# Kernel optimization log

Hardware: AMD Instinct MI355X
Metric: run time of the kernel (lower is better)

## Reference

```python
import jax, jax.numpy as jnp
import numpy as np

N_NODES = 50000
N_EDGES = 800000
DIN, EIN, DOUT, EOUT, H = 64, 32, 64, 64, 128


def mlp(x, W1, b1, W2, b2):
    # Linear -> ReLU -> Linear (assumed MLP definition, hidden=128)
    return jnp.dot(jax.nn.relu(jnp.dot(x, W1) + b1), W2) + b2


def setup_inputs() -> dict:
    key = jax.random.key(0)
    ks = jax.random.split(key, 18)
    init = lambda k, shape: (jax.random.normal(k, shape, dtype=jnp.float32)
                             / np.float32(np.sqrt(shape[0])))
    em_in = 2 * DIN + EIN   # 160
    nm_in = DIN + EOUT      # 128
    return {
        "nf": jax.random.normal(ks[0], (N_NODES, DIN), dtype=jnp.float32),
        "ef": jax.random.normal(ks[1], (N_EDGES, EIN), dtype=jnp.float32),
        "src": jax.random.randint(ks[2], (N_EDGES,), 0, N_NODES, dtype=jnp.int32),
        "dst": jax.random.randint(ks[3], (N_EDGES,), 0, N_NODES, dtype=jnp.int32),
        # edge model MLP
        "We1": init(ks[4], (em_in, H)), "be1": jnp.zeros((H,), jnp.float32),
        "We2": init(ks[5], (H, EOUT)), "be2": jnp.zeros((EOUT,), jnp.float32),
        # attention model MLP (scalar logit per edge)
        "Wa1": init(ks[6], (em_in, H)), "ba1": jnp.zeros((H,), jnp.float32),
        "Wa2": init(ks[7], (H, 1)), "ba2": jnp.zeros((1,), jnp.float32),
        # node model MLP
        "Wn1": init(ks[8], (nm_in, H)), "bn1": jnp.zeros((H,), jnp.float32),
        "Wn2": init(ks[9], (H, DOUT)), "bn2": jnp.zeros((DOUT,), jnp.float32),
    }


def reference(nf, ef, src, dst, We1, be1, We2, be2, Wa1, ba1, Wa2, ba2,
              Wn1, bn1, Wn2, bn2):
    # per-edge gather + concat: [E, 2*DIN + EIN]
    e_in = jnp.concatenate([nf[src], nf[dst], ef], axis=-1)
    uh_e = mlp(e_in, We1, be1, We2, be2)          # [E, EOUT]
    logits = mlp(e_in, Wa1, ba1, Wa2, ba2)        # [E, 1]
    # edge softmax over incoming edges of each destination node
    m = jax.ops.segment_max(logits, dst, num_segments=N_NODES)
    m = jnp.where(jnp.isfinite(m), m, jnp.float32(0.0))
    ex = jnp.exp(logits - m[dst])
    denom = jax.ops.segment_sum(ex, dst, num_segments=N_NODES)
    attn = ex / jnp.maximum(denom[dst], jnp.float32(1e-38))  # [E, 1]
    # attention-weighted scatter-sum aggregation
    agg = jax.ops.segment_sum(uh_e * attn, dst, num_segments=N_NODES)  # [N, EOUT]
    # node update MLP on concat(agg_m, nf)
    uh_n = mlp(jnp.concatenate([agg, nf], axis=-1), Wn1, bn1, Wn2, bn2)
    return (uh_n, uh_e)
```

## Files before the change

kernel.cpp:

```cpp
#include <hip/hip_runtime.h>


typedef unsigned short u16;
typedef __attribute__((ext_vector_type(8))) short bf16x8;
typedef __attribute__((ext_vector_type(4))) float f32x4;

#define NN 50000
#define NE 800000

__device__ __forceinline__ u16 f2bf(float f){
  union { float f; unsigned int i; } v; v.f = f;
  unsigned int i = v.i;
  return (u16)((i + 0x7FFFu + ((i >> 16) & 1u)) >> 16);
}
__device__ __forceinline__ uint2 f4tobf(float4 f){
  uint2 p;
  p.x = (unsigned)f2bf(f.x) | ((unsigned)f2bf(f.y) << 16);
  p.y = (unsigned)f2bf(f.z) | ((unsigned)f2bf(f.w) << 16);
  return p;
}

__global__ void prep_kernel(const float* __restrict__ We1, const float* __restrict__ Wa1,
                            const float* __restrict__ We2, const float* __restrict__ Wa2,
                            const float* __restrict__ Wn1, const float* __restrict__ Wn2,
                            u16* __restrict__ w1t, u16* __restrict__ w2t,
                            u16* __restrict__ wn1t, u16* __restrict__ wn2t,
                            int* __restrict__ head)
{
  int i = blockIdx.x * 256 + threadIdx.x;
  if (i < 40960) {
    int n = i / 160, k = i % 160;
    w1t[i] = f2bf((n < 128) ? We1[k*128 + n] : Wa1[k*128 + (n-128)]);
  } else if (i < 51200) {
    int j = i - 40960; int n = j / 128, k = j % 128;
    float v = (n < 64) ? We2[k*64 + n] : ((n == 64) ? Wa2[k] : 0.f);
    w2t[j] = f2bf(v);
  } else if (i < 67584) {
    int j = i - 51200; int n = j / 128, k = j % 128;
    wn1t[j] = f2bf(Wn1[k*128 + n]);
  } else if (i < 75776) {
    int j = i - 67584; int n = j / 128, k = j % 128;
    wn2t[j] = f2bf(Wn2[k*64 + n]);
  } else if (i < 125776) {
    head[i - 75776] = -1;
  }
}

__global__ void nfbf_kernel(const float* __restrict__ nf, u16* __restrict__ nfb)
{
  int i = blockIdx.x * 256 + threadIdx.x;
  if (i >= NN * 16) return;
  float4 f = *(const float4*)(nf + (size_t)i * 4);
  *(uint2*)&nfb[(size_t)i * 4] = f4tobf(f);
}

__global__ void link_kernel(const int* __restrict__ dst, int* __restrict__ head,
                            int* __restrict__ nxt)
{
  int e = blockIdx.x * 256 + threadIdx.x;
  if (e >= NE) return;
  nxt[e] = atomicExch(&head[dst[e]], e);
}

__global__ __launch_bounds__(256, 4) void edge_kernel(
    const u16* __restrict__ nfb, const float* __restrict__ ef,
    const int* __restrict__ src, const int* __restrict__ dst,
    const u16* __restrict__ w1t, const u16* __restrict__ w2t,
    const float* __restrict__ be1, const float* __restrict__ ba1,
    const float* __restrict__ be2, const float* __restrict__ ba2,
    float* __restrict__ uh_e, float* __restrict__ exu)
{
  __shared__ u16 smem[16896];
  __shared__ int s_src[64], s_dst[64];
  u16* eins = smem;
  u16* hsm  = smem;
  float* outs = (float*)smem;

  const int t = threadIdx.x;
  const int base = blockIdx.x * 64;

  if (t < 64)        s_src[t]      = src[base + t];
  else if (t < 128)  s_dst[t - 64] = dst[base + (t - 64)];
  __syncthreads();

  #pragma unroll
  for (int i = 0; i < 4; i++) {
    int idx = i*256 + t;
    int e = idx >> 4, c = idx & 15;
    uint2 v = *(const uint2*)(nfb + (size_t)s_src[e]*64 + c*4);
    *(uint2*)&eins[e*168 + c*4] = v;
  }
  #pragma unroll
  for (int i = 0; i < 4; i++) {
    int idx = i*256 + t;
    int e = idx >> 4, c = idx & 15;
    uint2 v = *(const uint2*)(nfb + (size_t)s_dst[e]*64 + c*4);
    *(uint2*)&eins[e*168 + 64 + c*4] = v;
  }
  #pragma unroll
  for (int i = 0; i < 2; i++) {
    int idx = i*256 + t;
    int e = idx >> 3, c = idx & 7;
    float4 f = *(const float4*)(ef + (size_t)(base + e)*32 + c*4);
    *(uint2*)&eins[e*168 + 128 + c*4] = f4tobf(f);
  }
  __syncthreads();

  const int lane = t & 63, wave = t >> 6;
  const int r = lane & 15, quad = lane >> 4;

  f32x4 acc[4][4];
  #pragma unroll
  for (int rf = 0; rf < 4; rf++)
    #pragma unroll
    for (int j = 0; j < 4; j++) acc[rf][j] = {0.f, 0.f, 0.f, 0.f};

  #pragma unroll
  for (int k0 = 0; k0 < 160; k0 += 32) {
    bf16x8 a[4];
    #pragma unroll
    for (int rf = 0; rf < 4; rf++)
      a[rf] = *(const bf16x8*)&eins[(rf*16 + r)*168 + k0 + quad*8];
    #pragma unroll
    for (int j = 0; j < 4; j++) {
      bf16x8 b = *(const bf16x8*)(w1t + (size_t)((wave*4 + j)*16 + r)*160 + k0 + quad*8);
      #pragma unroll
      for (int rf = 0; rf < 4; rf++)
        acc[rf][j] = __builtin_amdgcn_mfma_f32_16x16x32_bf16(a[rf], b, acc[rf][j], 0, 0, 0);
    }
  }
  __syncthreads();

  #pragma unroll
  for (int j = 0; j < 4; j++) {
    int col = (wave*4 + j)*16 + r;
    float bias = (wave < 2) ? be1[col] : ba1[col - 128];
    #pragma unroll
    for (int rf = 0; rf < 4; rf++)
      #pragma unroll
      for (int i = 0; i < 4; i++) {
        float h = fmaxf(acc[rf][j][i] + bias, 0.f);
        hsm[(rf*16 + quad*4 + i)*264 + col] = f2bf(h);
      }
  }
  __syncthreads();

  f32x4 acc2[4];
  f32x4 accl = {0.f, 0.f, 0.f, 0.f};
  #pragma unroll
  for (int rf = 0; rf < 4; rf++) acc2[rf] = {0.f, 0.f, 0.f, 0.f};

  #pragma unroll
  for (int k0 = 0; k0 < 128; k0 += 32) {
    bf16x8 bw = *(const bf16x8*)(w2t + (size_t)(wave*16 + r)*128 + k0 + quad*8);
    #pragma unroll
    for (int rf = 0; rf < 4; rf++) {
      bf16x8 ae = *(const bf16x8*)&hsm[(rf*16 + r)*264 + k0 + quad*8];
      acc2[rf] = __builtin_amdgcn_mfma_f32_16x16x32_bf16(ae, bw, acc2[rf], 0, 0, 0);
    }
    bf16x8 al = *(const bf16x8*)&hsm[(wave*16 + r)*264 + 128 + k0 + quad*8];
    bf16x8 bl = *(const bf16x8*)(w2t + (size_t)(64 + r)*128 + k0 + quad*8);
    accl = __builtin_amdgcn_mfma_f32_16x16x32_bf16(al, bl, accl, 0, 0, 0);
  }
  __syncthreads();

  {
    int col = wave*16 + r;
    float bias = be2[col];
    #pragma unroll
    for (int rf = 0; rf < 4; rf++)
      #pragma unroll
      for (int i = 0; i < 4; i++)
        outs[(rf*16 + quad*4 + i)*64 + col] = acc2[rf][i] + bias;
  }
  if (r == 0) {
    float bias = ba2[0];
    #pragma unroll
    for (int i = 0; i < 4; i++) {
      int row = wave*16 + quad*4 + i;
      float x = __expf(fminf(fmaxf(accl[i] + bias, -50.f), 50.f));
      exu[base + row] = x;
    }
  }
  __syncthreads();

  #pragma unroll
  for (int i = 0; i < 4; i++) {
    int idx = i*256 + t;
    int row = idx >> 4, c = idx & 15;
    *(float4*)(uh_e + (size_t)(base + row)*64 + c*4) = *(const float4*)&outs[row*64 + c*4];
  }
}

__global__ void agg_kernel(const int* __restrict__ head, const int* __restrict__ nxt,
                           const float* __restrict__ exu,
                           const float* __restrict__ uh_e, float* __restrict__ aggf)
{
  int gid = blockIdx.x * 256 + threadIdx.x;
  int v = gid >> 6, lane = gid & 63;
  if (v >= NN) return;
  float acc = 0.f, s = 0.f;
  int e = head[v];
  while (e >= 0) {
    float x = exu[e];
    s += x;
    acc += x * uh_e[(size_t)e*64 + lane];
    e = nxt[e];
  }
  aggf[(size_t)v*64 + lane] = acc / fmaxf(s, 1e-38f);
}

__global__ __launch_bounds__(256, 4) void node_kernel(
    const float* __restrict__ aggf, const float* __restrict__ nf,
    const u16* __restrict__ wn1t, const u16* __restrict__ wn2t,
    const float* __restrict__ bn1, const float* __restrict__ bn2,
    float* __restrict__ uh_n)
{
  __shared__ u16 smem[8704];
  u16* xs = smem;
  float* outs = (float*)smem;

  const int t = threadIdx.x;
  const int base = blockIdx.x * 64;

  #pragma unroll
  for (int i = 0; i < 8; i++) {
    int idx = i*256 + t;
    int row = idx >> 5, c = idx & 31;
    int v = base + row;
    float4 f = {0.f, 0.f, 0.f, 0.f};
    if (v < NN) {
      if (c < 16) f = *(const float4*)(aggf + (size_t)v*64 + c*4);
      else        f = *(const float4*)(nf   + (size_t)v*64 + (c-16)*4);
    }
    *(uint2*)&xs[row*136 + c*4] = f4tobf(f);
  }
  __syncthreads();

  const int lane = t & 63, wave = t >> 6;
  const int r = lane & 15, quad = lane >> 4;

  f32x4 acc1[8];
  #pragma unroll
  for (int i = 0; i < 8; i++) acc1[i] = {0.f, 0.f, 0.f, 0.f};
  #pragma unroll
  for (int k0 = 0; k0 < 128; k0 += 32) {
    bf16x8 a = *(const bf16x8*)&xs[(wave*16 + r)*136 + k0 + quad*8];
    #pragma unroll
    for (int tt = 0; tt < 8; tt++) {
      bf16x8 b = *(const bf16x8*)(wn1t + (size_t)(tt*16 + r)*128 + k0 + quad*8);
      acc1[tt] = __builtin_amdgcn_mfma_f32_16x16x32_bf16(a, b, acc1[tt], 0, 0, 0);
    }
  }
  __syncthreads();

  u16* hb = smem + wave*(16*136);
  #pragma unroll
  for (int tt = 0; tt < 8; tt++) {
    int col = tt*16 + r;
    float bias = bn1[col];
    #pragma unroll
    for (int i = 0; i < 4; i++) {
      float h = fmaxf(acc1[tt][i] + bias, 0.f);
      hb[(quad*4 + i)*136 + col] = f2bf(h);
    }
  }
  __syncthreads();

  f32x4 acc2[4];
  #pragma unroll
  for (int i = 0; i < 4; i++) acc2[i] = {0.f, 0.f, 0.f, 0.f};
  #pragma unroll
  for (int k0 = 0; k0 < 128; k0 += 32) {
    bf16x8 a = *(const bf16x8*)&hb[r*136 + k0 + quad*8];
    #pragma unroll
    for (int tt = 0; tt < 4; tt++) {
      bf16x8 b = *(const bf16x8*)(wn2t + (size_t)(tt*16 + r)*128 + k0 + quad*8);
      acc2[tt] = __builtin_amdgcn_mfma_f32_16x16x32_bf16(a, b, acc2[tt], 0, 0, 0);
    }
  }
  __syncthreads();

  #pragma unroll
  for (int tt = 0; tt < 4; tt++) {
    int col = tt*16 + r;
    float bias = bn2[col];
    #pragma unroll
    for (int i = 0; i < 4; i++)
      outs[(wave*16 + quad*4 + i)*64 + col] = acc2[tt][i] + bias;
  }
  __syncthreads();

  #pragma unroll
  for (int i = 0; i < 4; i++) {
    int idx = i*256 + t;
    int row = idx >> 4, c = idx & 15;
    int v2 = base + row;
    if (v2 < NN)
      *(float4*)(uh_n + (size_t)v2*64 + c*4) = *(const float4*)&outs[row*64 + c*4];
  }
}

extern "C" void kernel_launch(void* const* d_in, const int* in_sizes, int n_in,
                              void* d_out, int out_size, void* d_ws, size_t ws_size,
                              hipStream_t stream)
{
  const float* nf  = (const float*)d_in[0];
  const float* ef  = (const float*)d_in[1];
  const int*   src = (const int*)d_in[2];
  const int*   dst = (const int*)d_in[3];
  const float* We1 = (const float*)d_in[4];
  const float* be1 = (const float*)d_in[5];
  const float* We2 = (const float*)d_in[6];
  const float* be2 = (const float*)d_in[7];
  const float* Wa1 = (const float*)d_in[8];
  const float* ba1 = (const float*)d_in[9];
  const float* Wa2 = (const float*)d_in[10];
  const float* ba2 = (const float*)d_in[11];
  const float* Wn1 = (const float*)d_in[12];
  const float* bn1 = (const float*)d_in[13];
  const float* Wn2 = (const float*)d_in[14];
  const float* bn2 = (const float*)d_in[15];

  char* ws = (char*)d_ws;
  u16*   w1t    = (u16*)  (ws + 0);
  u16*   w2t    = (u16*)  (ws + 81920);
  u16*   wn1t   = (u16*)  (ws + 102400);
  u16*   wn2t   = (u16*)  (ws + 135168);
  float* exu    = (float*)(ws + 151552);
  int*   head   = (int*)  (ws + 3551552);
  int*   nxt    = (int*)  (ws + 3751552);

  float* uh_n = (float*)d_out;
  float* uh_e = (float*)d_out + (size_t)NN * 64;
  u16*   nfb  = (u16*)d_out;
  float* aggf = uh_n;

  prep_kernel<<<492, 256, 0, stream>>>(We1, Wa1, We2, Wa2, Wn1, Wn2,
                                       w1t, w2t, wn1t, wn2t, head);
  nfbf_kernel<<<3125, 256, 0, stream>>>(nf, nfb);
  link_kernel<<<(NE + 255)/256, 256, 0, stream>>>(dst, head, nxt);
  edge_kernel<<<NE/64, 256, 0, stream>>>(nfb, ef, src, dst, w1t, w2t,
                                         be1, ba1, be2, ba2, uh_e, exu);
  agg_kernel<<<(NN*64)/256, 256, 0, stream>>>(head, nxt, exu, uh_e, aggf);
  node_kernel<<<(NN + 63)/64, 256, 0, stream>>>(aggf, nf, wn1t, wn2t, bn1, bn2, uh_n);
}
```

Before: 649.7 us.

## Replace linked-list edge grouping with CSR build and persistent weight-resident edge kernel

```diff
diff --git a/kernel.cpp b/kernel.cpp
--- a/kernel.cpp
+++ b/kernel.cpp
@@ -25,7 +25,7 @@
                             const float* __restrict__ Wn1, const float* __restrict__ Wn2,
                             u16* __restrict__ w1t, u16* __restrict__ w2t,
                             u16* __restrict__ wn1t, u16* __restrict__ wn2t,
-                            int* __restrict__ head)
+                            int* __restrict__ deg)
 {
   int i = blockIdx.x * 256 + threadIdx.x;
   if (i < 40960) {
@@ -42,27 +42,69 @@
     int j = i - 67584; int n = j / 128, k = j % 128;
     wn2t[j] = f2bf(Wn2[k*64 + n]);
   } else if (i < 125776) {
-    head[i - 75776] = -1;
-  }
-}
-
-__global__ void nfbf_kernel(const float* __restrict__ nf, u16* __restrict__ nfb)
+    deg[i - 75776] = 0;
+  }
+}
+
+__global__ void deg_nfbf_kernel(const float* __restrict__ nf, u16* __restrict__ nfb,
+                                const int* __restrict__ dst, int* __restrict__ deg)
 {
   int i = blockIdx.x * 256 + threadIdx.x;
-  if (i >= NN * 16) return;
+  if (i >= NE) return;
   float4 f = *(const float4*)(nf + (size_t)i * 4);
   *(uint2*)&nfb[(size_t)i * 4] = f4tobf(f);
-}
-
-__global__ void link_kernel(const int* __restrict__ dst, int* __restrict__ head,
-                            int* __restrict__ nxt)
+  atomicAdd(&deg[dst[i]], 1);
+}
+
+__global__ void scan1_kernel(const int* __restrict__ deg, int* __restrict__ part,
+                             int* __restrict__ bsum)
+{
+  __shared__ int sm[256];
+  int t = threadIdx.x, g = blockIdx.x * 256 + t;
+  int x = (g < NN) ? deg[g] : 0;
+  sm[t] = x; __syncthreads();
+  #pragma unroll
+  for (int o = 1; o < 256; o <<= 1) {
+    int y = (t >= o) ? sm[t - o] : 0; __syncthreads();
+    sm[t] += y; __syncthreads();
+  }
+  if (g < NN) part[g] = sm[t] - x;
+  if (t == 255) bsum[blockIdx.x] = sm[255];
+}
+
+__global__ void scan2_kernel(int* __restrict__ bsum)
+{
+  __shared__ int sm[256];
+  int t = threadIdx.x;
+  int x = (t < 196) ? bsum[t] : 0;
+  sm[t] = x; __syncthreads();
+  #pragma unroll
+  for (int o = 1; o < 256; o <<= 1) {
+    int y = (t >= o) ? sm[t - o] : 0; __syncthreads();
+    sm[t] += y; __syncthreads();
+  }
+  if (t < 196) bsum[t] = sm[t] - x;
+}
+
+__global__ void scan3_kernel(const int* __restrict__ part, const int* __restrict__ bsum,
+                             int* __restrict__ rowptr, int* __restrict__ cursor)
+{
+  int g = blockIdx.x * 256 + threadIdx.x;
+  if (g >= NN) return;
+  int r = part[g] + bsum[blockIdx.x];
+  rowptr[g] = r; cursor[g] = r;
+}
+
+__global__ void fill_kernel(const int* __restrict__ dst, int* __restrict__ cursor,
+                            int* __restrict__ csr_e)
 {
   int e = blockIdx.x * 256 + threadIdx.x;
   if (e >= NE) return;
-  nxt[e] = atomicExch(&head[dst[e]], e);
-}
-
-__global__ __launch_bounds__(256, 4) void edge_kernel(
+  int slot = atomicAdd(&cursor[dst[e]], 1);
+  csr_e[slot] = e;
+}
+
+__global__ __launch_bounds__(256, 2) void edge_kernel(
     const u16* __restrict__ nfb, const float* __restrict__ ef,
     const int* __restrict__ src, const int* __restrict__ dst,
     const u16* __restrict__ w1t, const u16* __restrict__ w2t,
@@ -70,142 +112,162 @@
     const float* __restrict__ be2, const float* __restrict__ ba2,
     float* __restrict__ uh_e, float* __restrict__ exu)
 {
-  __shared__ u16 smem[16896];
-  __shared__ int s_src[64], s_dst[64];
-  u16* eins = smem;
-  u16* hsm  = smem;
-  float* outs = (float*)smem;
+  __shared__ u16 eins[64*168];
+  __shared__ u16 hsm [64*264];
+  __shared__ float outs[64*64];
 
   const int t = threadIdx.x;
-  const int base = blockIdx.x * 64;
-
-  if (t < 64)        s_src[t]      = src[base + t];
-  else if (t < 128)  s_dst[t - 64] = dst[base + (t - 64)];
-  __syncthreads();
-
-  #pragma unroll
-  for (int i = 0; i < 4; i++) {
-    int idx = i*256 + t;
-    int e = idx >> 4, c = idx & 15;
-    uint2 v = *(const uint2*)(nfb + (size_t)s_src[e]*64 + c*4);
-    *(uint2*)&eins[e*168 + c*4] = v;
-  }
-  #pragma unroll
-  for (int i = 0; i < 4; i++) {
-    int idx = i*256 + t;
-    int e = idx >> 4, c = idx & 15;
-    uint2 v = *(const uint2*)(nfb + (size_t)s_dst[e]*64 + c*4);
-    *(uint2*)&eins[e*168 + 64 + c*4] = v;
-  }
-  #pragma unroll
-  for (int i = 0; i < 2; i++) {
-    int idx = i*256 + t;
-    int e = idx >> 3, c = idx & 7;
-    float4 f = *(const float4*)(ef + (size_t)(base + e)*32 + c*4);
-    *(uint2*)&eins[e*168 + 128 + c*4] = f4tobf(f);
-  }
-  __syncthreads();
-
   const int lane = t & 63, wave = t >> 6;
   const int r = lane & 15, quad = lane >> 4;
 
-  f32x4 acc[4][4];
-  #pragma unroll
-  for (int rf = 0; rf < 4; rf++)
-    #pragma unroll
-    for (int j = 0; j < 4; j++) acc[rf][j] = {0.f, 0.f, 0.f, 0.f};
-
-  #pragma unroll
-  for (int k0 = 0; k0 < 160; k0 += 32) {
-    bf16x8 a[4];
-    #pragma unroll
-    for (int rf = 0; rf < 4; rf++)
-      a[rf] = *(const bf16x8*)&eins[(rf*16 + r)*168 + k0 + quad*8];
-    #pragma unroll
-    for (int j = 0; j < 4; j++) {
-      bf16x8 b = *(const bf16x8*)(w1t + (size_t)((wave*4 + j)*16 + r)*160 + k0 + quad*8);
-      #pragma unroll
-      for (int rf = 0; rf < 4; rf++)
-        acc[rf][j] = __builtin_amdgcn_mfma_f32_16x16x32_bf16(a[rf], b, acc[rf][j], 0, 0, 0);
-    }
-  }
-  __syncthreads();
-
+  bf16x8 wv1[5][4];
+  #pragma unroll
+  for (int k = 0; k < 5; k++)
+    #pragma unroll
+    for (int j = 0; j < 4; j++)
+      wv1[k][j] = *(const bf16x8*)(w1t + (size_t)((wave*4 + j)*16 + r)*160 + k*32 + quad*8);
+  bf16x8 wv2[4], wvl[4];
+  #pragma unroll
+  for (int k = 0; k < 4; k++) {
+    wv2[k] = *(const bf16x8*)(w2t + (size_t)(wave*16 + r)*128 + k*32 + quad*8);
+    wvl[k] = *(const bf16x8*)(w2t + (size_t)(64 + r)*128 + k*32 + quad*8);
+  }
+  float bias1[4];
   #pragma unroll
   for (int j = 0; j < 4; j++) {
     int col = (wave*4 + j)*16 + r;
-    float bias = (wave < 2) ? be1[col] : ba1[col - 128];
+    bias1[j] = (col < 128) ? be1[col] : ba1[col - 128];
+  }
+  const float bias2 = be2[wave*16 + r];
+  const float biasl = ba2[0];
+
+  for (int tt0 = 0; tt0 < 8; tt0++) {
+    int tile = blockIdx.x * 8 + tt0;
+    if (tile >= NE/64) break;
+    const int base = tile * 64;
+
+    #pragma unroll
+    for (int i = 0; i < 4; i++) {
+      int idx = i*256 + t;
+      int e = idx >> 4, c = idx & 15;
+      int sv = src[base + e];
+      *(uint2*)&eins[e*168 + c*4] = *(const uint2*)(nfb + (size_t)sv*64 + c*4);
+    }
+    #pragma unroll
+    for (int i = 0; i < 4; i++) {
+      int idx = i*256 + t;
+      int e = idx >> 4, c = idx & 15;
+      int dv = dst[base + e];
+      *(uint2*)&eins[e*168 + 64 + c*4] = *(const uint2*)(nfb + (size_t)dv*64 + c*4);
+    }
+    #pragma unroll
+    for (int i = 0; i < 2; i++) {
+      int idx = i*256 + t;
+      int e = idx >> 3, c = idx & 7;
+      float4 f = *(const float4*)(ef + (size_t)(base + e)*32 + c*4);
+      *(uint2*)&eins[e*168 + 128 + c*4] = f4tobf(f);
+    }
+    __syncthreads();
+
+    f32x4 acc[4][4];
     #pragma unroll
     for (int rf = 0; rf < 4; rf++)
       #pragma unroll
+      for (int j = 0; j < 4; j++) acc[rf][j] = {0.f, 0.f, 0.f, 0.f};
+
+    #pragma unroll
+    for (int k = 0; k < 5; k++) {
+      bf16x8 a[4];
+      #pragma unroll
+      for (int rf = 0; rf < 4; rf++)
+        a[rf] = *(const bf16x8*)&eins[(rf*16 + r)*168 + k*32 + quad*8];
+      #pragma unroll
+      for (int j = 0; j < 4; j++)
+        #pragma unroll
+        for (int rf = 0; rf < 4; rf++)
+          acc[rf][j] = __builtin_amdgcn_mfma_f32_16x16x32_bf16(a[rf], wv1[k][j], acc[rf][j], 0, 0, 0);
+    }
+
+    #pragma unroll
+    for (int j = 0; j < 4; j++) {
+      int col = (wave*4 + j)*16 + r;
+      #pragma unroll
+      for (int rf = 0; rf < 4; rf++)
+        #pragma unroll
+        for (int i = 0; i < 4; i++) {
+          float h = fmaxf(acc[rf][j][i] + bias1[j], 0.f);
+          hsm[(rf*16 + quad*4 + i)*264 + col] = f2bf(h);
+        }
+    }
+    __syncthreads();
+
+    f32x4 acc2[4];
+    f32x4 accl = {0.f, 0.f, 0.f, 0.f};
+    #pragma unroll
+    for (int rf = 0; rf < 4; rf++) acc2[rf] = {0.f, 0.f, 0.f, 0.f};
+    #pragma unroll
+    for (int k = 0; k < 4; k++) {
+      #pragma unroll
+      for (int rf = 0; rf < 4; rf++) {
+        bf16x8 ae = *(const bf16x8*)&hsm[(rf*16 + r)*264 + k*32 + quad*8];
+        acc2[rf] = __builtin_amdgcn_mfma_f32_16x16x32_bf16(ae, wv2[k], acc2[rf], 0, 0, 0);
+      }
+      bf16x8 al = *(const bf16x8*)&hsm[(wave*16 + r)*264 + 128 + k*32 + quad*8];
+      accl = __builtin_amdgcn_mfma_f32_16x16x32_bf16(al, wvl[k], accl, 0, 0, 0);
+    }
+
+    {
+      int col = wave*16 + r;
+      #pragma unroll
+      for (int rf = 0; rf < 4; rf++)
+        #pragma unroll
+        for (int i = 0; i < 4; i++)
+          outs[(rf*16 + quad*4 + i)*64 + col] = acc2[rf][i] + bias2;
+    }
+    if (r == 0) {
+      #pragma unroll
       for (int i = 0; i < 4; i++) {
-        float h = fmaxf(acc[rf][j][i] + bias, 0.f);
-        hsm[(rf*16 + quad*4 + i)*264 + col] = f2bf(h);
+        int row = wave*16 + quad*4 + i;
+        float x = __expf(fminf(fmaxf(accl[i] + biasl, -50.f), 50.f));
+        exu[base + row] = x;
       }
-  }
-  __syncthreads();
-
-  f32x4 acc2[4];
-  f32x4 accl = {0.f, 0.f, 0.f, 0.f};
-  #pragma unroll
-  for (int rf = 0; rf < 4; rf++) acc2[rf] = {0.f, 0.f, 0.f, 0.f};
-
-  #pragma unroll
-  for (int k0 = 0; k0 < 128; k0 += 32) {
-    bf16x8 bw = *(const bf16x8*)(w2t + (size_t)(wave*16 + r)*128 + k0 + quad*8);
-    #pragma unroll
-    for (int rf = 0; rf < 4; rf++) {
-      bf16x8 ae = *(const bf16x8*)&hsm[(rf*16 + r)*264 + k0 + quad*8];
-      acc2[rf] = __builtin_amdgcn_mfma_f32_16x16x32_bf16(ae, bw, acc2[rf], 0, 0, 0);
-    }
-    bf16x8 al = *(const bf16x8*)&hsm[(wave*16 + r)*264 + 128 + k0 + quad*8];
-    bf16x8 bl = *(const bf16x8*)(w2t + (size_t)(64 + r)*128 + k0 + quad*8);
-    accl = __builtin_amdgcn_mfma_f32_16x16x32_bf16(al, bl, accl, 0, 0, 0);
-  }
-  __syncthreads();
-
-  {
-    int col = wave*16 + r;
-    float bias = be2[col];
-    #pragma unroll
-    for (int rf = 0; rf < 4; rf++)
-      #pragma unroll
-      for (int i = 0; i < 4; i++)
-        outs[(rf*16 + quad*4 + i)*64 + col] = acc2[rf][i] + bias;
-  }
-  if (r == 0) {
-    float bias = ba2[0];
+    }
+    __syncthreads();
+
     #pragma unroll
     for (int i = 0; i < 4; i++) {
-      int row = wave*16 + quad*4 + i;
-      float x = __expf(fminf(fmaxf(accl[i] + bias, -50.f), 50.f));
-      exu[base + row] = x;
-    }
-  }
-  __syncthreads();
-
-  #pragma unroll
-  for (int i = 0; i < 4; i++) {
-    int idx = i*256 + t;
-    int row = idx >> 4, c = idx & 15;
-    *(float4*)(uh_e + (size_t)(base + row)*64 + c*4) = *(const float4*)&outs[row*64 + c*4];
-  }
-}
-
-__global__ void agg_kernel(const int* __restrict__ head, const int* __restrict__ nxt,
-                           const float* __restrict__ exu,
+      int idx = i*256 + t;
+      int row = idx >> 4, c = idx & 15;
+      *(float4*)(uh_e + (size_t)(base + row)*64 + c*4) = *(const float4*)&outs[row*64 + c*4];
+    }
+  }
+}
+
+__global__ void agg_kernel(const int* __restrict__ rowptr, const int* __restrict__ rowend,
+                           const int* __restrict__ csr_e, const float* __restrict__ exu,
                            const float* __restrict__ uh_e, float* __restrict__ aggf)
 {
   int gid = blockIdx.x * 256 + threadIdx.x;
   int v = gid >> 6, lane = gid & 63;
   if (v >= NN) return;
+  int beg = rowptr[v], end = rowend[v];
   float acc = 0.f, s = 0.f;
-  int e = head[v];
-  while (e >= 0) {
+  int i = beg;
+  for (; i + 4 <= end; i += 4) {
+    int e0 = csr_e[i], e1 = csr_e[i+1], e2 = csr_e[i+2], e3 = csr_e[i+3];
+    float x0 = exu[e0], x1 = exu[e1], x2 = exu[e2], x3 = exu[e3];
+    float u0 = uh_e[(size_t)e0*64 + lane];
+    float u1 = uh_e[(size_t)e1*64 + lane];
+    float u2 = uh_e[(size_t)e2*64 + lane];
+    float u3 = uh_e[(size_t)e3*64 + lane];
+    s += x0 + x1 + x2 + x3;
+    acc += x0*u0 + x1*u1 + x2*u2 + x3*u3;
+  }
+  for (; i < end; i++) {
+    int e = csr_e[i];
     float x = exu[e];
     s += x;
     acc += x * uh_e[(size_t)e*64 + lane];
-    e = nxt[e];
   }
   aggf[(size_t)v*64 + lane] = acc / fmaxf(s, 1e-38f);
 }
@@ -328,8 +390,12 @@
   u16*   wn1t   = (u16*)  (ws + 102400);
   u16*   wn2t   = (u16*)  (ws + 135168);
   float* exu    = (float*)(ws + 151552);
-  int*   head   = (int*)  (ws + 3551552);
-  int*   nxt    = (int*)  (ws + 3751552);
+  int*   deg    = (int*)  (ws + 3351552);
+  int*   part   = (int*)  (ws + 3551552);
+  int*   rowptr = (int*)  (ws + 3751552);
+  int*   cursor = (int*)  (ws + 3951552);
+  int*   bsum   = (int*)  (ws + 4151552);
+  int*   csr_e  = (int*)  (ws + 4152576);
 
   float* uh_n = (float*)d_out;
   float* uh_e = (float*)d_out + (size_t)NN * 64;
@@ -337,11 +403,14 @@
   float* aggf = uh_n;
 
   prep_kernel<<<492, 256, 0, stream>>>(We1, Wa1, We2, Wa2, Wn1, Wn2,
-                                       w1t, w2t, wn1t, wn2t, head);
-  nfbf_kernel<<<3125, 256, 0, stream>>>(nf, nfb);
-  link_kernel<<<(NE + 255)/256, 256, 0, stream>>>(dst, head, nxt);
-  edge_kernel<<<NE/64, 256, 0, stream>>>(nfb, ef, src, dst, w1t, w2t,
-                                         be1, ba1, be2, ba2, uh_e, exu);
-  agg_kernel<<<(NN*64)/256, 256, 0, stream>>>(head, nxt, exu, uh_e, aggf);
+                                       w1t, w2t, wn1t, wn2t, deg);
+  deg_nfbf_kernel<<<(NE + 255)/256, 256, 0, stream>>>(nf, nfb, dst, deg);
+  scan1_kernel<<<196, 256, 0, stream>>>(deg, part, bsum);
+  scan2_kernel<<<1, 256, 0, stream>>>(bsum);
+  scan3_kernel<<<196, 256, 0, stream>>>(part, bsum, rowptr, cursor);
+  fill_kernel<<<(NE + 255)/256, 256, 0, stream>>>(dst, cursor, csr_e);
+  edge_kernel<<<(NE/64 + 7)/8, 256, 0, stream>>>(nfb, ef, src, dst, w1t, w2t,
+                                                 be1, ba1, be2, ba2, uh_e, exu);
+  agg_kernel<<<(NN*64)/256, 256, 0, stream>>>(rowptr, cursor, csr_e, exu, uh_e, aggf);
   node_kernel<<<(NN + 63)/64, 256, 0, stream>>>(aggf, nf, wn1t, wn2t, bn1, bn2, uh_n);
 }
```

Result: slower. 822.8 us (+26.7%).

## Make edge kernel persistent over tiles with register-resident weights and prefetch

Applied to the files above, without the earlier changes.

```diff
diff --git a/kernel.cpp b/kernel.cpp
--- a/kernel.cpp
+++ b/kernel.cpp
@@ -7,6 +7,9 @@
 
 #define NN 50000
 #define NE 800000
+#define NT 12500
+#define TPB 8
+#define EGRID ((NT + TPB - 1) / TPB)
 
 __device__ __forceinline__ u16 f2bf(float f){
   union { float f; unsigned int i; } v; v.f = f;
@@ -62,7 +65,7 @@
   nxt[e] = atomicExch(&head[dst[e]], e);
 }
 
-__global__ __launch_bounds__(256, 4) void edge_kernel(
+__global__ __launch_bounds__(256, 1) void edge_kernel(
     const u16* __restrict__ nfb, const float* __restrict__ ef,
     const int* __restrict__ src, const int* __restrict__ dst,
     const u16* __restrict__ w1t, const u16* __restrict__ w2t,
@@ -71,124 +74,170 @@
     float* __restrict__ uh_e, float* __restrict__ exu)
 {
   __shared__ u16 smem[16896];
-  __shared__ int s_src[64], s_dst[64];
+  __shared__ float outs[64*64];
   u16* eins = smem;
   u16* hsm  = smem;
-  float* outs = (float*)smem;
 
   const int t = threadIdx.x;
-  const int base = blockIdx.x * 64;
-
-  if (t < 64)        s_src[t]      = src[base + t];
-  else if (t < 128)  s_dst[t - 64] = dst[base + (t - 64)];
-  __syncthreads();
-
-  #pragma unroll
-  for (int i = 0; i < 4; i++) {
-    int idx = i*256 + t;
-    int e = idx >> 4, c = idx & 15;
-    uint2 v = *(const uint2*)(nfb + (size_t)s_src[e]*64 + c*4);
-    *(uint2*)&eins[e*168 + c*4] = v;
-  }
-  #pragma unroll
-  for (int i = 0; i < 4; i++) {
-    int idx = i*256 + t;
-    int e = idx >> 4, c = idx & 15;
-    uint2 v = *(const uint2*)(nfb + (size_t)s_dst[e]*64 + c*4);
-    *(uint2*)&eins[e*168 + 64 + c*4] = v;
-  }
-  #pragma unroll
-  for (int i = 0; i < 2; i++) {
-    int idx = i*256 + t;
-    int e = idx >> 3, c = idx & 7;
-    float4 f = *(const float4*)(ef + (size_t)(base + e)*32 + c*4);
-    *(uint2*)&eins[e*168 + 128 + c*4] = f4tobf(f);
-  }
-  __syncthreads();
-
   const int lane = t & 63, wave = t >> 6;
   const int r = lane & 15, quad = lane >> 4;
 
-  f32x4 acc[4][4];
-  #pragma unroll
-  for (int rf = 0; rf < 4; rf++)
-    #pragma unroll
-    for (int j = 0; j < 4; j++) acc[rf][j] = {0.f, 0.f, 0.f, 0.f};
-
-  #pragma unroll
-  for (int k0 = 0; k0 < 160; k0 += 32) {
-    bf16x8 a[4];
-    #pragma unroll
-    for (int rf = 0; rf < 4; rf++)
-      a[rf] = *(const bf16x8*)&eins[(rf*16 + r)*168 + k0 + quad*8];
-    #pragma unroll
-    for (int j = 0; j < 4; j++) {
-      bf16x8 b = *(const bf16x8*)(w1t + (size_t)((wave*4 + j)*16 + r)*160 + k0 + quad*8);
-      #pragma unroll
-      for (int rf = 0; rf < 4; rf++)
-        acc[rf][j] = __builtin_amdgcn_mfma_f32_16x16x32_bf16(a[rf], b, acc[rf][j], 0, 0, 0);
-    }
-  }
-  __syncthreads();
-
+  const int tile0 = blockIdx.x * TPB;
+  const int ntiles = (NT - tile0 < TPB) ? (NT - tile0) : TPB;
+
+  bf16x8 wv1[5][4];
+  #pragma unroll
+  for (int k = 0; k < 5; k++)
+    #pragma unroll
+    for (int j = 0; j < 4; j++)
+      wv1[k][j] = *(const bf16x8*)(w1t + (size_t)((wave*4 + j)*16 + r)*160 + k*32 + quad*8);
+  bf16x8 wv2[4], wvl[4];
+  #pragma unroll
+  for (int k = 0; k < 4; k++) {
+    wv2[k] = *(const bf16x8*)(w2t + (size_t)(wave*16 + r)*128 + k*32 + quad*8);
+    wvl[k] = *(const bf16x8*)(w2t + (size_t)(64 + r)*128 + k*32 + quad*8);
+  }
+  float bias1[4];
   #pragma unroll
   for (int j = 0; j < 4; j++) {
     int col = (wave*4 + j)*16 + r;
-    float bias = (wave < 2) ? be1[col] : ba1[col - 128];
+    bias1[j] = (col < 128) ? be1[col] : ba1[col - 128];
+  }
+  const float bias2 = be2[wave*16 + r];
+  const float biasl = ba2[0];
+
+  uint2 gs[4], gd[4]; float4 gef[2];
+  {
+    const int nb = tile0 * 64;
+    #pragma unroll
+    for (int i = 0; i < 4; i++) {
+      int idx = i*256 + t, e = idx >> 4, c = idx & 15;
+      gs[i] = *(const uint2*)(nfb + (size_t)src[nb + e]*64 + c*4);
+      gd[i] = *(const uint2*)(nfb + (size_t)dst[nb + e]*64 + c*4);
+    }
+    #pragma unroll
+    for (int i = 0; i < 2; i++) {
+      int idx = i*256 + t, e = idx >> 3, c = idx & 7;
+      gef[i] = *(const float4*)(ef + (size_t)(nb + e)*32 + c*4);
+    }
+    #pragma unroll
+    for (int i = 0; i < 4; i++) {
+      int idx = i*256 + t, e = idx >> 4, c = idx & 15;
+      *(uint2*)&eins[e*168 + c*4]      = gs[i];
+      *(uint2*)&eins[e*168 + 64 + c*4] = gd[i];
+    }
+    #pragma unroll
+    for (int i = 0; i < 2; i++) {
+      int idx = i*256 + t, e = idx >> 3, c = idx & 7;
+      *(uint2*)&eins[e*168 + 128 + c*4] = f4tobf(gef[i]);
+    }
+  }
+  __syncthreads();
+
+  for (int tt = 0; tt < ntiles; tt++) {
+    const int nbase = (tile0 + tt) * 64;
+
+    if (tt + 1 < ntiles) {
+      const int nb = nbase + 64;
+      #pragma unroll
+      for (int i = 0; i < 4; i++) {
+        int idx = i*256 + t, e = idx >> 4, c = idx & 15;
+        gs[i] = *(const uint2*)(nfb + (size_t)src[nb + e]*64 + c*4);
+        gd[i] = *(const uint2*)(nfb + (size_t)dst[nb + e]*64 + c*4);
+      }
+      #pragma unroll
+      for (int i = 0; i < 2; i++) {
+        int idx = i*256 + t, e = idx >> 3, c = idx & 7;
+        gef[i] = *(const float4*)(ef + (size_t)(nb + e)*32 + c*4);
+      }
+    }
+
+    f32x4 acc[4][4];
     #pragma unroll
     for (int rf = 0; rf < 4; rf++)
       #pragma unroll
+      for (int j = 0; j < 4; j++) acc[rf][j] = {0.f, 0.f, 0.f, 0.f};
+
+    #pragma unroll
+    for (int k = 0; k < 5; k++) {
+      bf16x8 a[4];
+      #pragma unroll
+      for (int rf = 0; rf < 4; rf++)
+        a[rf] = *(const bf16x8*)&eins[(rf*16 + r)*168 + k*32 + quad*8];
+      #pragma unroll
+      for (int j = 0; j < 4; j++)
+        #pragma unroll
+        for (int rf = 0; rf < 4; rf++)
+          acc[rf][j] = __builtin_amdgcn_mfma_f32_16x16x32_bf16(a[rf], wv1[k][j], acc[rf][j], 0, 0, 0);
+    }
+    __syncthreads();
+
+    #pragma unroll
+    for (int j = 0; j < 4; j++) {
+      int col = (wave*4 + j)*16 + r;
+      #pragma unroll
+      for (int rf = 0; rf < 4; rf++)
+        #pragma unroll
+        for (int i = 0; i < 4; i++) {
+          float h = fmaxf(acc[rf][j][i] + bias1[j], 0.f);
+          hsm[(rf*16 + quad*4 + i)*264 + col] = f2bf(h);
+        }
+    }
+    __syncthreads();
+
+    f32x4 acc2[4];
+    f32x4 accl = {0.f, 0.f, 0.f, 0.f};
+    #pragma unroll
+    for (int rf = 0; rf < 4; rf++) acc2[rf] = {0.f, 0.f, 0.f, 0.f};
+    #pragma unroll
+    for (int k = 0; k < 4; k++) {
+      #pragma unroll
+      for (int rf = 0; rf < 4; rf++) {
+        bf16x8 ae = *(const bf16x8*)&hsm[(rf*16 + r)*264 + k*32 + quad*8];
+        acc2[rf] = __builtin_amdgcn_mfma_f32_16x16x32_bf16(ae, wv2[k], acc2[rf], 0, 0, 0);
+      }
+      bf16x8 al = *(const bf16x8*)&hsm[(wave*16 + r)*264 + 128 + k*32 + quad*8];
+      accl = __builtin_amdgcn_mfma_f32_16x16x32_bf16(al, wvl[k], accl, 0, 0, 0);
+    }
+    __syncthreads();
+
+    if (tt + 1 < ntiles) {
+      #pragma unroll
       for (int i = 0; i < 4; i++) {
-        float h = fmaxf(acc[rf][j][i] + bias, 0.f);
-        hsm[(rf*16 + quad*4 + i)*264 + col] = f2bf(h);
-      }
-  }
-  __syncthreads();
-
-  f32x4 acc2[4];
-  f32x4 accl = {0.f, 0.f, 0.f, 0.f};
-  #pragma unroll
-  for (int rf = 0; rf < 4; rf++) acc2[rf] = {0.f, 0.f, 0.f, 0.f};
-
-  #pragma unroll
-  for (int k0 = 0; k0 < 128; k0 += 32) {
-    bf16x8 bw = *(const bf16x8*)(w2t + (size_t)(wave*16 + r)*128 + k0 + quad*8);
-    #pragma unroll
-    for (int rf = 0; rf < 4; rf++) {
-      bf16x8 ae = *(const bf16x8*)&hsm[(rf*16 + r)*264 + k0 + quad*8];
-      acc2[rf] = __builtin_amdgcn_mfma_f32_16x16x32_bf16(ae, bw, acc2[rf], 0, 0, 0);
-    }
-    bf16x8 al = *(const bf16x8*)&hsm[(wave*16 + r)*264 + 128 + k0 + quad*8];
-    bf16x8 bl = *(const bf16x8*)(w2t + (size_t)(64 + r)*128 + k0 + quad*8);
-    accl = __builtin_amdgcn_mfma_f32_16x16x32_bf16(al, bl, accl, 0, 0, 0);
-  }
-  __syncthreads();
-
-  {
-    int col = wave*16 + r;
-    float bias = be2[col];
-    #pragma unroll
-    for (int rf = 0; rf < 4; rf++)
-      #pragma unroll
-      for (int i = 0; i < 4; i++)
-        outs[(rf*16 + quad*4 + i)*64 + col] = acc2[rf][i] + bias;
-  }
-  if (r == 0) {
-    float bias = ba2[0];
+        int idx = i*256 + t, e = idx >> 4, c = idx & 15;
+        *(uint2*)&eins[e*168 + c*4]      = gs[i];
+        *(uint2*)&eins[e*168 + 64 + c*4] = gd[i];
+      }
+      #pragma unroll
+      for (int i = 0; i < 2; i++) {
+        int idx = i*256 + t, e = idx >> 3, c = idx & 7;
+        *(uint2*)&eins[e*168 + 128 + c*4] = f4tobf(gef[i]);
+      }
+    }
+
+    {
+      int col = wave*16 + r;
+      #pragma unroll
+      for (int rf = 0; rf < 4; rf++)
+        #pragma unroll
+        for (int i = 0; i < 4; i++)
+          outs[(rf*16 + quad*4 + i)*64 + col] = acc2[rf][i] + bias2;
+    }
+    if (r == 0) {
+      #pragma unroll
+      for (int i = 0; i < 4; i++) {
+        int row = wave*16 + quad*4 + i;
+        float x = __expf(fminf(fmaxf(accl[i] + biasl, -50.f), 50.f));
+        exu[nbase + row] = x;
+      }
+    }
+    __syncthreads();
+
     #pragma unroll
     for (int i = 0; i < 4; i++) {
-      int row = wave*16 + quad*4 + i;
-      float x = __expf(fminf(fmaxf(accl[i] + bias, -50.f), 50.f));
-      exu[base + row] = x;
-    }
-  }
-  __syncthreads();
-
-  #pragma unroll
-  for (int i = 0; i < 4; i++) {
-    int idx = i*256 + t;
-    int row = idx >> 4, c = idx & 15;
-    *(float4*)(uh_e + (size_t)(base + row)*64 + c*4) = *(const float4*)&outs[row*64 + c*4];
+      int idx = i*256 + t, row = idx >> 4, c = idx & 15;
+      *(float4*)(uh_e + (size_t)(nbase + row)*64 + c*4) = *(const float4*)&outs[row*64 + c*4];
+    }
   }
 }
 
@@ -216,9 +265,9 @@
     const float* __restrict__ bn1, const float* __restrict__ bn2,
     float* __restrict__ uh_n)
 {
-  __shared__ u16 smem[8704];
-  u16* xs = smem;
-  float* outs = (float*)smem;
+  __shared__ u16 smem2[8704];
+  u16* xs = smem2;
+  float* outs = (float*)smem2;
 
   const int t = threadIdx.x;
   const int base = blockIdx.x * 64;
@@ -254,7 +303,7 @@
   }
   __syncthreads();
 
-  u16* hb = smem + wave*(16*136);
+  u16* hb = smem2 + wave*(16*136);
   #pragma unroll
   for (int tt = 0; tt < 8; tt++) {
     int col = tt*16 + r;
@@ -340,7 +389,7 @@
                                        w1t, w2t, wn1t, wn2t, head);
   nfbf_kernel<<<3125, 256, 0, stream>>>(nf, nfb);
   link_kernel<<<(NE + 255)/256, 256, 0, stream>>>(dst, head, nxt);
-  edge_kernel<<<NE/64, 256, 0, stream>>>(nfb, ef, src, dst, w1t, w2t,
+  edge_kernel<<<EGRID, 256, 0, stream>>>(nfb, ef, src, dst, w1t, w2t,
                                          be1, ba1, be2, ba2, uh_e, exu);
   agg_kernel<<<(NN*64)/256, 256, 0, stream>>>(head, nxt, exu, uh_e, aggf);
   node_kernel<<<(NN + 63)/64, 256, 0, stream>>>(aggf, nf, wn1t, wn2t, bn1, bn2, uh_n);
```

After: 646.9 us. No clear change (-0.4%).
